# Optimization experiments

Measured on AMD Instinct MI355X. Metric: run time of the kernel, lower is better.

The kernel has to match this reference:

```python
import jax, jax.numpy as jnp
import numpy as np

N = 50000        # nodes
E = 800000       # edges
IN_C = 128       # in_channels
HID = 256        # hidden_channels
HEADS = 4
HD = HID // HEADS
LAYERS = 4
GRAPHS = 64
OUT_C = 32
MAX_POS = 10
EPS = 1e-5


def layer_norm(x, g, b):
    mu = jnp.mean(x, axis=-1, keepdims=True)
    var = jnp.mean((x - mu) ** 2, axis=-1, keepdims=True)
    return (x - mu) / jnp.sqrt(var + EPS) * g + b


def setup_inputs() -> dict:
    key = jax.random.key(0)
    ks = jax.random.split(key, 32)
    s = 0.02
    inp = {
        "x": jax.random.normal(ks[0], (N, IN_C), dtype=jnp.float32),
        "edge_index": jax.random.randint(ks[1], (2, E), 0, N, dtype=jnp.int32),
        "pos_idx": jax.random.randint(ks[2], (N,), 0, MAX_POS, dtype=jnp.int32),
        "batch": jnp.sort(jax.random.randint(ks[3], (N,), 0, GRAPHS, dtype=jnp.int32)),
        # encoder MLP: Linear(IN->HID), ReLU, LN(HID), Linear(HID->HID); weights stored [in,out]
        "enc_w1": jax.random.normal(ks[4], (IN_C, HID)) * s,
        "enc_b1": jnp.zeros((HID,), jnp.float32),
        "enc_g": jnp.ones((HID,), jnp.float32),
        "enc_beta": jnp.zeros((HID,), jnp.float32),
        "enc_w2": jax.random.normal(ks[5], (HID, HID)) * s,
        "enc_b2": jnp.zeros((HID,), jnp.float32),
        "pos_emb": jax.random.normal(ks[6], (MAX_POS, HID)) * s,
        # stacked attention-layer params [LAYERS, ...]
        "Wq": jax.random.normal(ks[7], (LAYERS, HID, HID)) * s,
        "bq": jnp.zeros((LAYERS, HID), jnp.float32),
        "Wk": jax.random.normal(ks[8], (LAYERS, HID, HID)) * s,
        "bk": jnp.zeros((LAYERS, HID), jnp.float32),
        "Wv": jax.random.normal(ks[9], (LAYERS, HID, HID)) * s,
        "bv": jnp.zeros((LAYERS, HID), jnp.float32),
        "mlp_w1": jax.random.normal(ks[10], (LAYERS, 2 * HID, HID)) * s,
        "mlp_b1": jnp.zeros((LAYERS, HID), jnp.float32),
        "mlp_g": jnp.ones((LAYERS, HID), jnp.float32),
        "mlp_beta": jnp.zeros((LAYERS, HID), jnp.float32),
        "mlp_w2": jax.random.normal(ks[11], (LAYERS, HID, HID)) * s,
        "mlp_b2": jnp.zeros((LAYERS, HID), jnp.float32),
        # classifier
        "cls_w1": jax.random.normal(ks[12], (HID, HID)) * s,
        "cls_b1": jnp.zeros((HID,), jnp.float32),
        "cls_g": jnp.ones((HID,), jnp.float32),
        "cls_beta": jnp.zeros((HID,), jnp.float32),
        "cls_w2": jax.random.normal(ks[13], (HID, OUT_C)) * s,
        "cls_b2": jnp.zeros((OUT_C,), jnp.float32),
    }
    return inp


def reference(x, edge_index, pos_idx, batch,
              enc_w1, enc_b1, enc_g, enc_beta, enc_w2, enc_b2, pos_emb,
              Wq, bq, Wk, bk, Wv, bv,
              mlp_w1, mlp_b1, mlp_g, mlp_beta, mlp_w2, mlp_b2,
              cls_w1, cls_b1, cls_g, cls_beta, cls_w2, cls_b2):
    row, col = edge_index[0], edge_index[1]
    n = x.shape[0]
    e = row.shape[0]

    # NodeEncoder
    h = layer_norm(jax.nn.relu(x @ enc_w1 + enc_b1), enc_g, enc_beta) @ enc_w2 + enc_b2
    h = h + pos_emb[pos_idx]

    scale = jnp.asarray(HD, h.dtype) ** 0.5
    for l in range(LAYERS):
        Q = (h @ Wq[l] + bq[l]).reshape(n, HEADS, HD)
        K = (h @ Wk[l] + bk[l]).reshape(n, HEADS, HD)
        V = (h @ Wv[l] + bv[l]).reshape(n, HEADS, HD)
        # per-edge attention scores [E, HEADS]
        scores = jnp.sum(Q[row] * K[col], axis=-1) / scale
        # segment softmax over destination node `row`
        m = jax.ops.segment_max(scores, row, num_segments=n)
        ex = jnp.exp(scores - m[row])
        denom = jax.ops.segment_sum(ex, row, num_segments=n)
        w = ex / denom[row]                         # [E, HEADS]
        msg = (w[..., None] * V[col]).reshape(e, HID)
        agg = jax.ops.segment_sum(msg, row, num_segments=n)  # [N, HID]
        cat = jnp.concatenate([h, agg], axis=-1)
        z = layer_norm(jax.nn.relu(cat @ mlp_w1[l] + mlp_b1[l]), mlp_g[l], mlp_beta[l]) @ mlp_w2[l] + mlp_b2[l]
        h = z + h

    # global mean pool over graphs
    sums = jax.ops.segment_sum(h, batch, num_segments=GRAPHS)
    cnt = jax.ops.segment_sum(jnp.ones((n, 1), h.dtype), batch, num_segments=GRAPHS)
    pooled = sums / jnp.maximum(cnt, 1.0)

    out = layer_norm(jax.nn.relu(pooled @ cls_w1 + cls_b1), cls_g, cls_beta) @ cls_w2 + cls_b2
    return out
```

## Files before the change

### kernel.cpp

```cpp
#include <hip/hip_runtime.h>
#include <cstdint>

#define HID 256
#define HEADS 4
#define GRAPHS 64
#define OUTC 32
#define EPSV 1e-5f
#define PSPLIT 32

typedef __bf16 b16x8 __attribute__((ext_vector_type(8)));
typedef float  f32x4 __attribute__((ext_vector_type(4)));

__device__ __forceinline__ f32x4 mfma16(b16x8 a, b16x8 b, f32x4 c) {
    return __builtin_amdgcn_mfma_f32_16x16x32_bf16(a, b, c, 0, 0, 0);
}

__device__ __forceinline__ unsigned int pack_bf16(float a, float b) {
    unsigned short ua = __builtin_bit_cast(unsigned short, (__bf16)a);
    unsigned short ub = __builtin_bit_cast(unsigned short, (__bf16)b);
    return (unsigned int)ua | ((unsigned int)ub << 16);
}

__device__ __forceinline__ void unpack2(unsigned int u, float& lo, float& hi) {
    lo = __builtin_bit_cast(float, u << 16);
    hi = __builtin_bit_cast(float, u & 0xffff0000u);
}

__device__ __forceinline__ float b2f(unsigned short u) {
    return __builtin_bit_cast(float, (unsigned int)u << 16);
}

__device__ __forceinline__ void stage_gld128(char* buf, const unsigned short* __restrict__ src,
                                             int base, int tid)
{
#pragma unroll
    for (int i = 0; i < 16; i++) {
        int idx = i * 256 + tid;
        int r = idx >> 5;
        int u = idx & 31;
        int us = u ^ (r & 7);
        const void* gp = (const void*)(src + (size_t)(base + r) * HID + us * 8);
        __builtin_amdgcn_global_load_lds(
            (const __attribute__((address_space(1))) void*)gp,
            (__attribute__((address_space(3))) void*)(buf + idx * 16),
            16, 0, 0);
    }
}

__global__ __launch_bounds__(256) void wtrans_all(
    const float* __restrict__ e1, const float* __restrict__ e2,
    const float* __restrict__ q,  const float* __restrict__ k,
    const float* __restrict__ v,  const float* __restrict__ m1,
    const float* __restrict__ m2,
    unsigned short* __restrict__ we1, unsigned short* __restrict__ we2,
    unsigned short* __restrict__ wq,  unsigned short* __restrict__ wk,
    unsigned short* __restrict__ wv,  unsigned short* __restrict__ wm1,
    unsigned short* __restrict__ wm2)
{
    __shared__ float tile[32][33];
    int z = blockIdx.z;
    const float* W; unsigned short* Wt; int K; int mat = 0;
    if (z == 0)      { W = e1; Wt = we1; K = 128; }
    else if (z == 1) { W = e2; Wt = we2; K = 256; }
    else if (z < 6)  { W = q;  Wt = wq;  K = 256; mat = z - 2; }
    else if (z < 10) { W = k;  Wt = wk;  K = 256; mat = z - 6; }
    else if (z < 14) { W = v;  Wt = wv;  K = 256; mat = z - 10; }
    else if (z < 18) { W = m1; Wt = wm1; K = 512; mat = z - 14; }
    else             { W = m2; Wt = wm2; K = 256; mat = z - 18; }
    int k0 = blockIdx.x * 32;
    if (k0 >= K) return;
    const int C = 256;
    W  += (size_t)mat * K * C;
    Wt += (size_t)mat * K * C;
    int c0 = blockIdx.y * 32;
    int tx = threadIdx.x & 31, ty = threadIdx.x >> 5;
#pragma unroll
    for (int i = 0; i < 32; i += 8)
        tile[ty + i][tx] = W[(size_t)(k0 + ty + i) * C + c0 + tx];
    __syncthreads();
#pragma unroll
    for (int i = 0; i < 32; i += 8) {
        float vv = tile[tx][ty + i];
        Wt[(size_t)(c0 + ty + i) * K + k0 + tx] =
            __builtin_bit_cast(unsigned short, (__bf16)vv);
    }
}

__global__ __launch_bounds__(256) void enc1_mfma(
    const float* __restrict__ in0, const unsigned short* __restrict__ Wt,
    const float* __restrict__ bias, const float* __restrict__ g,
    const float* __restrict__ be, unsigned short* __restrict__ outb, int n)
{
    constexpr int KTILE = 128, ROWB = 256;
    __shared__ __align__(16) char alds[64 * 256];
    __shared__ float red[4][64][2];
    int tid = threadIdx.x, lane = tid & 63, wv = tid >> 6;
    int cg = lane & 15, rg = lane >> 4;
    int base = blockIdx.x * 64;
    int cbase = wv * 64;

    f32x4 acc[4][4];
#pragma unroll
    for (int m = 0; m < 4; m++)
#pragma unroll
        for (int f = 0; f < 4; f++) acc[m][f] = (f32x4){0.f, 0.f, 0.f, 0.f};

#pragma unroll
    for (int i = 0; i < 8; i++) {
        int idx = (i * 256 + tid) * 4;
        int row = idx >> 7, k = idx & 127;
        int node = base + row;
        float4 v = {0.f, 0.f, 0.f, 0.f};
        if (node < n) v = *(const float4*)(in0 + (size_t)node * KTILE + k);
        uint2 pp; pp.x = pack_bf16(v.x, v.y); pp.y = pack_bf16(v.z, v.w);
        int off = row * ROWB + k * 2;
        off ^= (row & 7) << 4;
        *(uint2*)(alds + off) = pp;
    }
    __syncthreads();

#pragma unroll 2
    for (int k0 = 0; k0 < KTILE; k0 += 32) {
        b16x8 a[4], b[4];
#pragma unroll
        for (int m = 0; m < 4; m++) {
            int R = m * 16 + cg;
            int off = R * ROWB + (k0 + rg * 8) * 2;
            off ^= (R & 7) << 4;
            a[m] = __builtin_bit_cast(b16x8, *(const uint4*)(alds + off));
        }
#pragma unroll
        for (int f = 0; f < 4; f++) {
            const unsigned short* p = Wt + (size_t)(cbase + f * 16 + cg) * KTILE + k0 + rg * 8;
            b[f] = __builtin_bit_cast(b16x8, *(const uint4*)p);
        }
#pragma unroll
        for (int m = 0; m < 4; m++)
#pragma unroll
            for (int f = 0; f < 4; f++)
                acc[m][f] = mfma16(a[m], b[f], acc[m][f]);
    }

    float bias_v[4], g_v[4], be_v[4];
#pragma unroll
    for (int f = 0; f < 4; f++) {
        int col = cbase + f * 16 + cg;
        bias_v[f] = bias[col]; g_v[f] = g[col]; be_v[f] = be[col];
    }
#pragma unroll
    for (int m = 0; m < 4; m++)
#pragma unroll
        for (int f = 0; f < 4; f++)
#pragma unroll
            for (int r = 0; r < 4; r++)
                acc[m][f][r] = fmaxf(acc[m][f][r] + bias_v[f], 0.f);
#pragma unroll
    for (int m = 0; m < 4; m++)
#pragma unroll
        for (int r = 0; r < 4; r++) {
            float s = acc[m][0][r] + acc[m][1][r] + acc[m][2][r] + acc[m][3][r];
            float q = acc[m][0][r] * acc[m][0][r] + acc[m][1][r] * acc[m][1][r]
                    + acc[m][2][r] * acc[m][2][r] + acc[m][3][r] * acc[m][3][r];
#pragma unroll
            for (int o = 1; o < 16; o <<= 1) {
                s += __shfl_xor(s, o, 64); q += __shfl_xor(q, o, 64);
            }
            if (cg == 0) { int R = m * 16 + rg * 4 + r; red[wv][R][0] = s; red[wv][R][1] = q; }
        }
    __syncthreads();
#pragma unroll
    for (int m = 0; m < 4; m++)
#pragma unroll
        for (int r = 0; r < 4; r++) {
            int R = m * 16 + rg * 4 + r;
            float S = red[0][R][0] + red[1][R][0] + red[2][R][0] + red[3][R][0];
            float Q = red[0][R][1] + red[1][R][1] + red[2][R][1] + red[3][R][1];
            float mu = S * (1.f / HID);
            float rs = rsqrtf(Q * (1.f / HID) - mu * mu + EPSV);
            int row = base + R;
            if (row >= n) continue;
            size_t ro = (size_t)row * HID;
#pragma unroll
            for (int f = 0; f < 4; f++) {
                float v = (acc[m][f][r] - mu) * rs * g_v[f] + be_v[f];
                outb[ro + cbase + f * 16 + cg] = __builtin_bit_cast(unsigned short, (__bf16)v);
            }
        }
}

template<int NPASS, bool RELU_LN, bool ADD_RES, bool POS>
__global__ __launch_bounds__(256) void gemm128(
    const unsigned short* __restrict__ in0, const unsigned short* __restrict__ in1,
    const unsigned short* __restrict__ Wt, const float* __restrict__ bias,
    const float* __restrict__ g, const float* __restrict__ be,
    const unsigned short* __restrict__ addsrc, const float* __restrict__ pos_emb,
    const int* __restrict__ pidx, unsigned short* __restrict__ outb, int n)
{
    constexpr int KS = 256 * NPASS;
    __shared__ __align__(16) char alds[128 * 512];
    __shared__ float red[4][128][2];

    int tid = threadIdx.x, lane = tid & 63, wv = tid >> 6;
    int cg = lane & 15, rg = lane >> 4;
    int base = blockIdx.x * 128;
    int cbase = wv * 64;

    f32x4 acc[2][4][4];
#pragma unroll
    for (int t = 0; t < 2; t++)
#pragma unroll
        for (int m = 0; m < 4; m++)
#pragma unroll
            for (int f = 0; f < 4; f++) acc[t][m][f] = (f32x4){0.f, 0.f, 0.f, 0.f};

    for (int pass = 0; pass < NPASS; pass++) {
        if (pass) __syncthreads();
        const unsigned short* src = pass ? in1 : in0;
        const unsigned short* Wp = Wt + pass * 256;

        stage_gld128(alds, src, base, tid);
        __syncthreads();

#pragma unroll
        for (int kk = 0; kk < 8; kk++) {
            b16x8 b[4];
#pragma unroll
            for (int f = 0; f < 4; f++)
                b[f] = __builtin_bit_cast(b16x8, *(const uint4*)(
                    Wp + (size_t)(cbase + f * 16 + cg) * KS + kk * 32 + rg * 8));
#pragma unroll
            for (int t = 0; t < 2; t++) {
                b16x8 a[4];
#pragma unroll
                for (int m = 0; m < 4; m++) {
                    int R = t * 64 + m * 16 + cg;
                    int off = R * 512 + (kk * 32 + rg * 8) * 2;
                    off ^= (R & 7) << 4;
                    a[m] = __builtin_bit_cast(b16x8, *(const uint4*)(alds + off));
                }
#pragma unroll
                for (int m = 0; m < 4; m++)
#pragma unroll
                    for (int f = 0; f < 4; f++)
                        acc[t][m][f] = mfma16(a[m], b[f], acc[t][m][f]);
            }
        }
    }

    float bias_v[4], g_v[4], be_v[4];
#pragma unroll
    for (int f = 0; f < 4; f++) {
        int col = cbase + f * 16 + cg;
        bias_v[f] = bias[col];
        if (RELU_LN) { g_v[f] = g[col]; be_v[f] = be[col]; }
    }
#pragma unroll
    for (int t = 0; t < 2; t++)
#pragma unroll
        for (int m = 0; m < 4; m++)
#pragma unroll
            for (int f = 0; f < 4; f++)
#pragma unroll
                for (int r = 0; r < 4; r++) acc[t][m][f][r] += bias_v[f];

    if (RELU_LN) {
#pragma unroll
        for (int t = 0; t < 2; t++)
#pragma unroll
            for (int m = 0; m < 4; m++)
#pragma unroll
                for (int f = 0; f < 4; f++)
#pragma unroll
                    for (int r = 0; r < 4; r++)
                        acc[t][m][f][r] = fmaxf(acc[t][m][f][r], 0.f);
#pragma unroll
        for (int t = 0; t < 2; t++)
#pragma unroll
            for (int m = 0; m < 4; m++)
#pragma unroll
                for (int r = 0; r < 4; r++) {
                    float s = acc[t][m][0][r] + acc[t][m][1][r] + acc[t][m][2][r] + acc[t][m][3][r];
                    float q = acc[t][m][0][r] * acc[t][m][0][r] + acc[t][m][1][r] * acc[t][m][1][r]
                            + acc[t][m][2][r] * acc[t][m][2][r] + acc[t][m][3][r] * acc[t][m][3][r];
#pragma unroll
                    for (int o = 1; o < 16; o <<= 1) {
                        s += __shfl_xor(s, o, 64); q += __shfl_xor(q, o, 64);
                    }
                    if (cg == 0) {
                        int R = t * 64 + m * 16 + rg * 4 + r;
                        red[wv][R][0] = s; red[wv][R][1] = q;
                    }
                }
        __syncthreads();
#pragma unroll
        for (int t = 0; t < 2; t++)
#pragma unroll
            for (int m = 0; m < 4; m++)
#pragma unroll
                for (int r = 0; r < 4; r++) {
                    int R = t * 64 + m * 16 + rg * 4 + r;
                    float S = red[0][R][0] + red[1][R][0] + red[2][R][0] + red[3][R][0];
                    float Q = red[0][R][1] + red[1][R][1] + red[2][R][1] + red[3][R][1];
                    float mu = S * (1.f / HID);
                    float rs = rsqrtf(Q * (1.f / HID) - mu * mu + EPSV);
#pragma unroll
                    for (int f = 0; f < 4; f++)
                        acc[t][m][f][r] = (acc[t][m][f][r] - mu) * rs * g_v[f] + be_v[f];
                }
    }

#pragma unroll
    for (int t = 0; t < 2; t++)
#pragma unroll
        for (int m = 0; m < 4; m++)
#pragma unroll
            for (int r = 0; r < 4; r++) {
                int row = base + t * 64 + m * 16 + rg * 4 + r;
                if (row >= n) continue;
                size_t ro = (size_t)row * HID;
                int pid = 0;
                if (POS) pid = pidx[row];
#pragma unroll
                for (int f = 0; f < 4; f++) {
                    int col = cbase + f * 16 + cg;
                    float v = acc[t][m][f][r];
                    if (ADD_RES) v += b2f(addsrc[ro + col]);
                    if (POS)     v += pos_emb[(size_t)pid * HID + col];
                    outb[ro + col] = __builtin_bit_cast(unsigned short, (__bf16)v);
                }
            }
}

__global__ __launch_bounds__(256) void mlp_fused(
    const unsigned short* __restrict__ h16, const unsigned short* __restrict__ a16,
    const unsigned short* __restrict__ Wt1, const float* __restrict__ b1,
    const float* __restrict__ g, const float* __restrict__ be,
    const unsigned short* __restrict__ Wt2, const float* __restrict__ b2,
    unsigned short* __restrict__ hout, int n)
{
    __shared__ __align__(16) char alds[128 * 512];
    __shared__ float red[4][128][2];
    int tid = threadIdx.x, lane = tid & 63, wv = tid >> 6;
    int cg = lane & 15, rg = lane >> 4;
    int base = blockIdx.x * 128;
    int cbase = wv * 64;

    f32x4 acc[2][4][4];
#pragma unroll
    for (int t = 0; t < 2; t++)
#pragma unroll
        for (int m = 0; m < 4; m++)
#pragma unroll
            for (int f = 0; f < 4; f++) acc[t][m][f] = (f32x4){0.f, 0.f, 0.f, 0.f};

    for (int pass = 0; pass < 2; pass++) {
        if (pass) __syncthreads();
        const unsigned short* src = pass ? a16 : h16;
        const unsigned short* Wp = Wt1 + pass * 256;
        stage_gld128(alds, src, base, tid);
        __syncthreads();
#pragma unroll
        for (int kk = 0; kk < 8; kk++) {
            b16x8 b[4];
#pragma unroll
            for (int f = 0; f < 4; f++)
                b[f] = __builtin_bit_cast(b16x8, *(const uint4*)(
                    Wp + (size_t)(cbase + f * 16 + cg) * 512 + kk * 32 + rg * 8));
#pragma unroll
            for (int t = 0; t < 2; t++) {
                b16x8 a[4];
#pragma unroll
                for (int m = 0; m < 4; m++) {
                    int R = t * 64 + m * 16 + cg;
                    int off = R * 512 + (kk * 32 + rg * 8) * 2;
                    off ^= (R & 7) << 4;
                    a[m] = __builtin_bit_cast(b16x8, *(const uint4*)(alds + off));
                }
#pragma unroll
                for (int m = 0; m < 4; m++)
#pragma unroll
                    for (int f = 0; f < 4; f++)
                        acc[t][m][f] = mfma16(a[m], b[f], acc[t][m][f]);
            }
        }
    }

    float b1_v[4], g_v[4], be_v[4];
#pragma unroll
    for (int f = 0; f < 4; f++) {
        int col = cbase + f * 16 + cg;
        b1_v[f] = b1[col]; g_v[f] = g[col]; be_v[f] = be[col];
    }
#pragma unroll
    for (int t = 0; t < 2; t++)
#pragma unroll
        for (int m = 0; m < 4; m++)
#pragma unroll
            for (int f = 0; f < 4; f++)
#pragma unroll
                for (int r = 0; r < 4; r++)
                    acc[t][m][f][r] = fmaxf(acc[t][m][f][r] + b1_v[f], 0.f);
#pragma unroll
    for (int t = 0; t < 2; t++)
#pragma unroll
        for (int m = 0; m < 4; m++)
#pragma unroll
            for (int r = 0; r < 4; r++) {
                float s = acc[t][m][0][r] + acc[t][m][1][r] + acc[t][m][2][r] + acc[t][m][3][r];
                float q = acc[t][m][0][r] * acc[t][m][0][r] + acc[t][m][1][r] * acc[t][m][1][r]
                        + acc[t][m][2][r] * acc[t][m][2][r] + acc[t][m][3][r] * acc[t][m][3][r];
#pragma unroll
                for (int o = 1; o < 16; o <<= 1) {
                    s += __shfl_xor(s, o, 64); q += __shfl_xor(q, o, 64);
                }
                if (cg == 0) {
                    int R = t * 64 + m * 16 + rg * 4 + r;
                    red[wv][R][0] = s; red[wv][R][1] = q;
                }
            }
    __syncthreads();
#pragma unroll
    for (int t = 0; t < 2; t++)
#pragma unroll
        for (int m = 0; m < 4; m++)
#pragma unroll
            for (int r = 0; r < 4; r++) {
                int R = t * 64 + m * 16 + rg * 4 + r;
                float S = red[0][R][0] + red[1][R][0] + red[2][R][0] + red[3][R][0];
                float Q = red[0][R][1] + red[1][R][1] + red[2][R][1] + red[3][R][1];
                float mu = S * (1.f / HID);
                float rs = rsqrtf(Q * (1.f / HID) - mu * mu + EPSV);
#pragma unroll
                for (int f = 0; f < 4; f++)
                    acc[t][m][f][r] = (acc[t][m][f][r] - mu) * rs * g_v[f] + be_v[f];
            }

    __syncthreads();
#pragma unroll
    for (int t = 0; t < 2; t++)
#pragma unroll
        for (int m = 0; m < 4; m++)
#pragma unroll
            for (int r = 0; r < 4; r++) {
                int R = t * 64 + m * 16 + rg * 4 + r;
#pragma unroll
                for (int f = 0; f < 4; f++) {
                    int col = cbase + f * 16 + cg;
                    int off = R * 512 + col * 2;
                    off ^= (R & 7) << 4;
                    *(unsigned short*)(alds + off) =
                        __builtin_bit_cast(unsigned short, (__bf16)acc[t][m][f][r]);
                }
            }
    __syncthreads();

#pragma unroll
    for (int t = 0; t < 2; t++)
#pragma unroll
        for (int m = 0; m < 4; m++)
#pragma unroll
            for (int f = 0; f < 4; f++) acc[t][m][f] = (f32x4){0.f, 0.f, 0.f, 0.f};
#pragma unroll
    for (int kk = 0; kk < 8; kk++) {
        b16x8 b[4];
#pragma unroll
        for (int f = 0; f < 4; f++)
            b[f] = __builtin_bit_cast(b16x8, *(const uint4*)(
                Wt2 + (size_t)(cbase + f * 16 + cg) * 256 + kk * 32 + rg * 8));
#pragma unroll
        for (int t = 0; t < 2; t++) {
            b16x8 a[4];
#pragma unroll
            for (int m = 0; m < 4; m++) {
                int R = t * 64 + m * 16 + cg;
                int off = R * 512 + (kk * 32 + rg * 8) * 2;
                off ^= (R & 7) << 4;
                a[m] = __builtin_bit_cast(b16x8, *(const uint4*)(alds + off));
            }
#pragma unroll
            for (int m = 0; m < 4; m++)
#pragma unroll
                for (int f = 0; f < 4; f++)
                    acc[t][m][f] = mfma16(a[m], b[f], acc[t][m][f]);
        }
    }

    float b2_v[4];
#pragma unroll
    for (int f = 0; f < 4; f++) b2_v[f] = b2[cbase + f * 16 + cg];
#pragma unroll
    for (int t = 0; t < 2; t++)
#pragma unroll
        for (int m = 0; m < 4; m++)
#pragma unroll
            for (int r = 0; r < 4; r++) {
                int row = base + t * 64 + m * 16 + rg * 4 + r;
                if (row >= n) continue;
                size_t ro = (size_t)row * HID;
#pragma unroll
                for (int f = 0; f < 4; f++) {
                    int col = cbase + f * 16 + cg;
                    float v = acc[t][m][f][r] + b2_v[f] + b2f(hout[ro + col]);
                    hout[ro + col] = __builtin_bit_cast(unsigned short, (__bf16)v);
                }
            }
}

__global__ __launch_bounds__(256) void qkv128_kernel(
    const unsigned short* __restrict__ hsrc,
    const unsigned short* __restrict__ Wtq, const unsigned short* __restrict__ Wtk,
    const unsigned short* __restrict__ Wtv,
    const float* __restrict__ bq, const float* __restrict__ bk, const float* __restrict__ bv,
    unsigned short* __restrict__ Qo, unsigned short* __restrict__ KVo, int n)
{
    __shared__ __align__(16) char alds[128 * 512];
    int tid = threadIdx.x, lane = tid & 63, wv = tid >> 6;
    int cg = lane & 15, rg = lane >> 4;
    int base = blockIdx.x * 128;
    int cbase = wv * 64;
    int mat = blockIdx.y;
    const unsigned short* Wp = (mat == 0) ? Wtq : (mat == 1) ? Wtk : Wtv;
    const float* bp = (mat == 0) ? bq : (mat == 1) ? bk : bv;
    unsigned short* op = (mat == 0) ? Qo : KVo;
    int ostride = (mat == 0) ? HID : 512;
    int coff = (mat == 2) ? 256 : 0;

    stage_gld128(alds, hsrc, base, tid);
    __syncthreads();

    f32x4 acc[2][4][4];
#pragma unroll
    for (int t = 0; t < 2; t++)
#pragma unroll
        for (int m = 0; m < 4; m++)
#pragma unroll
            for (int f = 0; f < 4; f++) acc[t][m][f] = (f32x4){0.f, 0.f, 0.f, 0.f};

#pragma unroll
    for (int kk = 0; kk < 8; kk++) {
        b16x8 b[4];
#pragma unroll
        for (int f = 0; f < 4; f++)
            b[f] = __builtin_bit_cast(b16x8, *(const uint4*)(
                Wp + (size_t)(cbase + f * 16 + cg) * 256 + kk * 32 + rg * 8));
#pragma unroll
        for (int t = 0; t < 2; t++) {
            b16x8 a[4];
#pragma unroll
            for (int m = 0; m < 4; m++) {
                int R = t * 64 + m * 16 + cg;
                int off = R * 512 + (kk * 32 + rg * 8) * 2;
                off ^= (R & 7) << 4;
                a[m] = __builtin_bit_cast(b16x8, *(const uint4*)(alds + off));
            }
#pragma unroll
            for (int m = 0; m < 4; m++)
#pragma unroll
                for (int f = 0; f < 4; f++)
                    acc[t][m][f] = mfma16(a[m], b[f], acc[t][m][f]);
        }
    }

    float bias_v[4];
#pragma unroll
    for (int f = 0; f < 4; f++) bias_v[f] = bp[cbase + f * 16 + cg];
#pragma unroll
    for (int t = 0; t < 2; t++)
#pragma unroll
        for (int m = 0; m < 4; m++)
#pragma unroll
            for (int r = 0; r < 4; r++) {
                int row = base + t * 64 + m * 16 + rg * 4 + r;
                if (row >= n) continue;
                size_t ro = (size_t)row * ostride + coff;
#pragma unroll
                for (int f = 0; f < 4; f++) {
                    float v = acc[t][m][f][r] + bias_v[f];
                    op[ro + cbase + f * 16 + cg] =
                        __builtin_bit_cast(unsigned short, (__bf16)v);
                }
            }
}

__global__ void count_kernel(const int* __restrict__ row, int* __restrict__ counts, int e)
{
    int i = blockIdx.x * blockDim.x + threadIdx.x;
    if (i < e) atomicAdd(&counts[row[i]], 1);
}

__global__ __launch_bounds__(256) void scan1_kernel(const int* __restrict__ counts,
    int* __restrict__ offs, int* __restrict__ bsum, int n)
{
    __shared__ int wsumS[4];
    int tid = threadIdx.x, b = blockIdx.x;
    int i = b * 256 + tid;
    int v = (i < n) ? counts[i] : 0;
    int lane = tid & 63, wv = tid >> 6;
    int s = v;
#pragma unroll
    for (int o = 1; o < 64; o <<= 1) { int t = __shfl_up(s, o, 64); if (lane >= o) s += t; }
    if (lane == 63) wsumS[wv] = s;
    __syncthreads();
    int add = 0;
    for (int j = 0; j < wv; j++) add += wsumS[j];
    s += add;
    if (i < n) offs[i + 1] = s;
    if (tid == 255) bsum[b] = s;
}

__global__ __launch_bounds__(256) void scan2_kernel(int* __restrict__ bsum, int nb)
{
    __shared__ int wsumS[4];
    int tid = threadIdx.x;
    int v = (tid < nb) ? bsum[tid] : 0;
    int lane = tid & 63, wv = tid >> 6;
    int s = v;
#pragma unroll
    for (int o = 1; o < 64; o <<= 1) { int t = __shfl_up(s, o, 64); if (lane >= o) s += t; }
    if (lane == 63) wsumS[wv] = s;
    __syncthreads();
    int add = 0;
    for (int j = 0; j < wv; j++) add += wsumS[j];
    s += add;
    if (tid < nb) bsum[tid] = s;
}

__global__ __launch_bounds__(256) void scan3_kernel(int* __restrict__ offs,
    const int* __restrict__ bsum, int n)
{
    int tid = threadIdx.x, b = blockIdx.x;
    int i = b * 256 + tid;
    if (i == 0) offs[0] = 0;
    if (i < n && b > 0) offs[i + 1] += bsum[b - 1];
}

__global__ void scatter_kernel(const int* __restrict__ row, const int* __restrict__ col,
    const int* __restrict__ offs, int* __restrict__ cur, int* __restrict__ ccol, int e)
{
    int i = blockIdx.x * blockDim.x + threadIdx.x;
    if (i >= e) return;
    int r = row[i];
    int pos = atomicAdd(&cur[r], 1);
    ccol[offs[r] + pos] = col[i];
}

__global__ __launch_bounds__(256) void attn_fw_kernel(
    const unsigned short* __restrict__ Qm, const unsigned short* __restrict__ KV,
    const int* __restrict__ offs, const int* __restrict__ ccol,
    unsigned short* __restrict__ agg, int n)
{
    int tid = threadIdx.x;
    int wv = tid >> 6;
    int lane = tid & 63;
    int half = lane >> 5;
    int l32 = lane & 31;
    int node = blockIdx.x * 4 + wv;
    if (node >= n) return;
    int start = offs[node], fin = offs[node + 1];
    size_t rowoff = (size_t)node * HID + l32 * 8;
    if (start == fin) {
        if (half == 0) {
            uint4 z = {0u, 0u, 0u, 0u};
            *(uint4*)(agg + rowoff) = z;
        }
        return;
    }

    uint4 qr = *(const uint4*)(Qm + rowoff);
    float qf[8];
    unpack2(qr.x, qf[0], qf[1]);
    unpack2(qr.y, qf[2], qf[3]);
    unpack2(qr.z, qf[4], qf[5]);
    unpack2(qr.w, qf[6], qf[7]);

    float m = -3.0e38f, d = 0.f;
    float acc[8];
#pragma unroll
    for (int j = 0; j < 8; j++) acc[j] = 0.f;

    for (int i = start + half; i < fin; i += 2) {
        int c = ccol[i];
        const unsigned short* kvp = KV + (size_t)c * 512 + l32 * 8;
        uint4 kr = *(const uint4*)kvp;
        uint4 vr = *(const uint4*)(kvp + 256);
        float k0, k1, k2, k3, k4, k5, k6, k7;
        unpack2(kr.x, k0, k1); unpack2(kr.y, k2, k3);
        unpack2(kr.z, k4, k5); unpack2(kr.w, k6, k7);
        float p = qf[0] * k0 + qf[1] * k1 + qf[2] * k2 + qf[3] * k3
                + qf[4] * k4 + qf[5] * k5 + qf[6] * k6 + qf[7] * k7;
        p += __shfl_xor(p, 1, 64);
        p += __shfl_xor(p, 2, 64);
        p += __shfl_xor(p, 4, 64);
        float s = p * 0.125f;
        float mn = fmaxf(m, s);
        float sc = __expf(m - mn);
        float w = __expf(s - mn);
        d = d * sc + w;
        float v0, v1, v2, v3, v4, v5, v6, v7;
        unpack2(vr.x, v0, v1); unpack2(vr.y, v2, v3);
        unpack2(vr.z, v4, v5); unpack2(vr.w, v6, v7);
        acc[0] = acc[0] * sc + w * v0;  acc[1] = acc[1] * sc + w * v1;
        acc[2] = acc[2] * sc + w * v2;  acc[3] = acc[3] * sc + w * v3;
        acc[4] = acc[4] * sc + w * v4;  acc[5] = acc[5] * sc + w * v5;
        acc[6] = acc[6] * sc + w * v6;  acc[7] = acc[7] * sc + w * v7;
        m = mn;
    }

    float mo = __shfl_xor(m, 32, 64);
    float M = fmaxf(m, mo);
    float fs = __expf(m - M);
    float fo = __expf(mo - M);
    float D = d * fs + __shfl_xor(d, 32, 64) * fo;
    float inv = 1.f / D;
#pragma unroll
    for (int j = 0; j < 8; j++) {
        float other = __shfl_xor(acc[j], 32, 64);
        acc[j] = (acc[j] * fs + other * fo) * inv;
    }

    if (half == 0) {
        uint4 out;
        out.x = pack_bf16(acc[0], acc[1]);
        out.y = pack_bf16(acc[2], acc[3]);
        out.z = pack_bf16(acc[4], acc[5]);
        out.w = pack_bf16(acc[6], acc[7]);
        *(uint4*)(agg + rowoff) = out;
    }
}

__global__ void bounds_kernel(const int* __restrict__ batch, int* __restrict__ gb, int n)
{
    int g = threadIdx.x;
    if (g > GRAPHS) return;
    int lo = 0, hi = n;
    while (lo < hi) { int mid = (lo + hi) >> 1; if (batch[mid] < g) lo = mid + 1; else hi = mid; }
    gb[g] = lo;
}

__global__ __launch_bounds__(256) void pool_partial_kernel(
    const unsigned short* __restrict__ h16,
    const int* __restrict__ gb, float* __restrict__ partial)
{
    int s = blockIdx.x, g = blockIdx.y, tid = threadIdx.x;
    int lo = gb[g], hi = gb[g + 1];
    float sum = 0.f;
    for (int i = lo + s; i < hi; i += PSPLIT)
        sum += b2f(h16[(size_t)i * HID + tid]);
    partial[((size_t)g * PSPLIT + s) * HID + tid] = sum;
}

__global__ __launch_bounds__(256) void pool_reduce_kernel(const float* __restrict__ partial,
    const int* __restrict__ gb, float* __restrict__ pooled)
{
    int g = blockIdx.x, tid = threadIdx.x;
    float sum = 0.f;
#pragma unroll
    for (int s = 0; s < PSPLIT; s++) sum += partial[((size_t)g * PSPLIT + s) * HID + tid];
    int cnt = gb[g + 1] - gb[g];
    pooled[g * HID + tid] = sum / fmaxf((float)cnt, 1.f);
}

__global__ __launch_bounds__(256) void cls_kernel(const float* __restrict__ pooled,
    const float* __restrict__ W1, const float* __restrict__ b1,
    const float* __restrict__ g, const float* __restrict__ be,
    const float* __restrict__ W2, const float* __restrict__ b2,
    float* __restrict__ out)
{
    __shared__ float pin[HID];
    __shared__ float hbuf[HID];
    __shared__ float red2[4][2];
    int tid = threadIdx.x, gi = blockIdx.x;
    int lane = tid & 63, wv = tid >> 6;
    pin[tid] = pooled[gi * HID + tid];
    __syncthreads();
    float acc = 0.f;
    for (int k = 0; k < HID; k++) acc += pin[k] * W1[k * HID + tid];
    acc = fmaxf(acc + b1[tid], 0.f);
    float s = acc, q = acc * acc;
#pragma unroll
    for (int o = 1; o < 64; o <<= 1) { s += __shfl_xor(s, o, 64); q += __shfl_xor(q, o, 64); }
    if (lane == 0) { red2[wv][0] = s; red2[wv][1] = q; }
    __syncthreads();
    float S = red2[0][0] + red2[1][0] + red2[2][0] + red2[3][0];
    float Q = red2[0][1] + red2[1][1] + red2[2][1] + red2[3][1];
    float mu = S * (1.f / HID);
    float rs = rsqrtf(Q * (1.f / HID) - mu * mu + EPSV);
    hbuf[tid] = (acc - mu) * rs * g[tid] + be[tid];
    __syncthreads();
    if (tid < OUTC) {
        float o = 0.f;
        for (int k = 0; k < HID; k++) o += hbuf[k] * W2[k * OUTC + tid];
        out[gi * OUTC + tid] = o + b2[tid];
    }
}

extern "C" void kernel_launch(void* const* d_in, const int* in_sizes, int n_in,
                              void* d_out, int out_size, void* d_ws, size_t ws_size,
                              hipStream_t stream)
{
    const float* x        = (const float*)d_in[0];
    const int*   ei       = (const int*)d_in[1];
    const int*   pidx     = (const int*)d_in[2];
    const int*   batch    = (const int*)d_in[3];
    const float* enc_w1   = (const float*)d_in[4];
    const float* enc_b1   = (const float*)d_in[5];
    const float* enc_g    = (const float*)d_in[6];
    const float* enc_beta = (const float*)d_in[7];
    const float* enc_w2   = (const float*)d_in[8];
    const float* enc_b2   = (const float*)d_in[9];
    const float* pos_emb  = (const float*)d_in[10];
    const float* Wq       = (const float*)d_in[11];
    const float* bq       = (const float*)d_in[12];
    const float* Wk       = (const float*)d_in[13];
    const float* bk       = (const float*)d_in[14];
    const float* Wv       = (const float*)d_in[15];
    const float* bv       = (const float*)d_in[16];
    const float* mlp_w1   = (const float*)d_in[17];
    const float* mlp_b1   = (const float*)d_in[18];
    const float* mlp_g    = (const float*)d_in[19];
    const float* mlp_beta = (const float*)d_in[20];
    const float* mlp_w2   = (const float*)d_in[21];
    const float* mlp_b2   = (const float*)d_in[22];
    const float* cls_w1   = (const float*)d_in[23];
    const float* cls_b1   = (const float*)d_in[24];
    const float* cls_g    = (const float*)d_in[25];
    const float* cls_beta = (const float*)d_in[26];
    const float* cls_w2   = (const float*)d_in[27];
    const float* cls_b2   = (const float*)d_in[28];

    int n = in_sizes[2];
    int e = in_sizes[1] / 2;
    const int* row = ei;
    const int* col = ei + e;

    char* p = (char*)d_ws;
    auto alloc = [&](size_t bytes) -> void* {
        void* r = (void*)p;
        p += (bytes + 255) & ~(size_t)255;
        return r;
    };
    size_t NH = (size_t)n * HID;
    unsigned short* h16  = (unsigned short*)alloc(NH * 2);
    unsigned short* a16  = (unsigned short*)alloc(NH * 2);
    unsigned short* m16  = (unsigned short*)alloc(NH * 2);
    unsigned short* Qb   = (unsigned short*)alloc(NH * 2);
    unsigned short* KVb  = (unsigned short*)alloc(NH * 4);
    float* partial = (float*)alloc((size_t)GRAPHS * PSPLIT * HID * 4);
    float* pooled  = (float*)alloc((size_t)GRAPHS * HID * 4);
    int* counts = (int*)alloc((size_t)n * 4);
    int* offs   = (int*)alloc((size_t)(n + 1) * 4);
    int* cur    = (int*)alloc((size_t)n * 4);
    int* ccol   = (int*)alloc((size_t)e * 4);
    int* bsum   = (int*)alloc(1024);
    int* gb     = (int*)alloc((GRAPHS + 1) * 4);
    unsigned short* wt_e1 = (unsigned short*)alloc((size_t)128 * 256 * 2);
    unsigned short* wt_e2 = (unsigned short*)alloc((size_t)256 * 256 * 2);
    unsigned short* wt_q  = (unsigned short*)alloc((size_t)4 * 256 * 256 * 2);
    unsigned short* wt_k  = (unsigned short*)alloc((size_t)4 * 256 * 256 * 2);
    unsigned short* wt_v  = (unsigned short*)alloc((size_t)4 * 256 * 256 * 2);
    unsigned short* wt_m1 = (unsigned short*)alloc((size_t)4 * 512 * 256 * 2);
    unsigned short* wt_m2 = (unsigned short*)alloc((size_t)4 * 256 * 256 * 2);

    int gblocks64  = (n + 63) / 64;
    int gblocks128 = (n + 127) / 128;
    int nb = (n + 255) / 256;

    wtrans_all<<<dim3(16, 8, 22), 256, 0, stream>>>(
        enc_w1, enc_w2, Wq, Wk, Wv, mlp_w1, mlp_w2,
        wt_e1, wt_e2, wt_q, wt_k, wt_v, wt_m1, wt_m2);

    hipMemsetAsync(counts, 0, (size_t)n * 4, stream);
    hipMemsetAsync(cur, 0, (size_t)n * 4, stream);
    count_kernel<<<(e + 255) / 256, 256, 0, stream>>>(row, counts, e);
    scan1_kernel<<<nb, 256, 0, stream>>>(counts, offs, bsum, n);
    scan2_kernel<<<1, 256, 0, stream>>>(bsum, nb);
    scan3_kernel<<<nb, 256, 0, stream>>>(offs, bsum, n);
    scatter_kernel<<<(e + 255) / 256, 256, 0, stream>>>(row, col, offs, cur, ccol, e);
    bounds_kernel<<<1, 128, 0, stream>>>(batch, gb, n);

    enc1_mfma<<<gblocks64, 256, 0, stream>>>(x, wt_e1, enc_b1, enc_g, enc_beta, m16, n);
    gemm128<1, false, false, true><<<gblocks128, 256, 0, stream>>>(
        m16, nullptr, wt_e2, enc_b2, nullptr, nullptr, nullptr, pos_emb, pidx, h16, n);

    int ablocks = (n + 3) / 4;
    for (int l = 0; l < 4; l++) {
        size_t wo = (size_t)l * 256 * 256;
        size_t bo = (size_t)l * HID;
        qkv128_kernel<<<dim3(gblocks128, 3), 256, 0, stream>>>(
            h16, wt_q + wo, wt_k + wo, wt_v + wo, bq + bo, bk + bo, bv + bo,
            Qb, KVb, n);
        attn_fw_kernel<<<ablocks, 256, 0, stream>>>(Qb, KVb, offs, ccol, a16, n);
        mlp_fused<<<gblocks128, 256, 0, stream>>>(
            h16, a16, wt_m1 + (size_t)l * 512 * 256, mlp_b1 + bo,
            mlp_g + bo, mlp_beta + bo, wt_m2 + wo, mlp_b2 + bo, h16, n);
    }

    pool_partial_kernel<<<dim3(PSPLIT, GRAPHS), 256, 0, stream>>>(h16, gb, partial);
    pool_reduce_kernel<<<GRAPHS, 256, 0, stream>>>(partial, gb, pooled);
    cls_kernel<<<GRAPHS, 256, 0, stream>>>(pooled, cls_w1, cls_b1, cls_g, cls_beta,
                                           cls_w2, cls_b2, (float*)d_out);
}
```

Before: 1.168 ms.

## Double-buffer LDS staging of MLP input in 128-column K chunks

Splits the 512-wide K loop of the fused MLP kernel into four 128-column chunks staged into two 32KB LDS halves. The next chunk is prefetched with global_load_lds while MFMAs run on the current one, replacing the old stage-then-compute-per-pass scheme. The goal is to hide global-to-LDS latency behind compute. In exchange it adds a barrier per chunk and keeps more outstanding loads in flight alongside the accumulators.

```diff
diff --git a/kernel.cpp b/kernel.cpp
--- a/kernel.cpp
+++ b/kernel.cpp
@@ -40,6 +40,23 @@
         int u = idx & 31;
         int us = u ^ (r & 7);
         const void* gp = (const void*)(src + (size_t)(base + r) * HID + us * 8);
+        __builtin_amdgcn_global_load_lds(
+            (const __attribute__((address_space(1))) void*)gp,
+            (__attribute__((address_space(3))) void*)(buf + idx * 16),
+            16, 0, 0);
+    }
+}
+
+__device__ __forceinline__ void stage_half(char* buf, const unsigned short* __restrict__ src,
+                                           int base, int colbase, int tid)
+{
+#pragma unroll
+    for (int i = 0; i < 8; i++) {
+        int idx = i * 256 + tid;
+        int r = idx >> 4;
+        int u = idx & 15;
+        int us = u ^ (r & 7);
+        const void* gp = (const void*)(src + (size_t)(base + r) * HID + colbase + us * 8);
         __builtin_amdgcn_global_load_lds(
             (const __attribute__((address_space(1))) void*)gp,
             (__attribute__((address_space(3))) void*)(buf + idx * 16),
@@ -353,28 +370,33 @@
 #pragma unroll
             for (int f = 0; f < 4; f++) acc[t][m][f] = (f32x4){0.f, 0.f, 0.f, 0.f};
 
-    for (int pass = 0; pass < 2; pass++) {
-        if (pass) __syncthreads();
-        const unsigned short* src = pass ? a16 : h16;
-        const unsigned short* Wp = Wt1 + pass * 256;
-        stage_gld128(alds, src, base, tid);
-        __syncthreads();
-#pragma unroll
-        for (int kk = 0; kk < 8; kk++) {
+    stage_half(alds, h16, base, 0, tid);
+    __syncthreads();
+
+#pragma unroll
+    for (int ht = 0; ht < 4; ht++) {
+        if (ht < 3) {
+            const unsigned short* s = (ht + 1 < 2) ? h16 : a16;
+            int cb = ((ht + 1) & 1) * 128;
+            stage_half(alds + (((ht + 1) & 1) << 15), s, base, cb, tid);
+        }
+        const char* buf = alds + ((ht & 1) << 15);
+#pragma unroll
+        for (int kk = 0; kk < 4; kk++) {
             b16x8 b[4];
 #pragma unroll
             for (int f = 0; f < 4; f++)
                 b[f] = __builtin_bit_cast(b16x8, *(const uint4*)(
-                    Wp + (size_t)(cbase + f * 16 + cg) * 512 + kk * 32 + rg * 8));
+                    Wt1 + (size_t)(cbase + f * 16 + cg) * 512 + ht * 128 + kk * 32 + rg * 8));
 #pragma unroll
             for (int t = 0; t < 2; t++) {
                 b16x8 a[4];
 #pragma unroll
                 for (int m = 0; m < 4; m++) {
                     int R = t * 64 + m * 16 + cg;
-                    int off = R * 512 + (kk * 32 + rg * 8) * 2;
+                    int off = R * 256 + (kk * 32 + rg * 8) * 2;
                     off ^= (R & 7) << 4;
-                    a[m] = __builtin_bit_cast(b16x8, *(const uint4*)(alds + off));
+                    a[m] = __builtin_bit_cast(b16x8, *(const uint4*)(buf + off));
                 }
 #pragma unroll
                 for (int m = 0; m < 4; m++)
@@ -383,6 +405,7 @@
                         acc[t][m][f] = mfma16(a[m], b[f], acc[t][m][f]);
             }
         }
+        __syncthreads();
     }
 
     float b1_v[4], g_v[4], be_v[4];
```

New measurement: 1.161 ms. No clear change (-0.6%).
